# Kernel tuning notes

Hardware: AMD Instinct MI355X
Metric: run time of the kernel (lower is better)

Reference implementation:

```python
import math
import jax, jax.numpy as jnp
import numpy as np

# Dimensions (scalar irreps: o3.Irreps('8x0e').dim == 8, FullyConnectedTensorProduct
# between scalar irreps reduces to a learned bilinear map with a 3D weight tensor)
N = 50000       # nodes
C = 4           # channel dim ('c' in the einsum 'nci,neio->nceo')
DI = 8          # irreps_in.dim
DE = 8          # irreps_edge_attr.dim (must equal DI for the einsum to typecheck)
DO = 8          # irreps_out.dim (must equal DI for lin2 to consume the messages)
DA = 16         # irreps_node_attr.dim
E = 400000      # edges
F_EDGE = 32     # number_of_edge_features
H = 64          # radial_neurons
NUM_NEIGHBORS = 8


def setup_inputs() -> dict:
    key = jax.random.key(0)
    ks = jax.random.split(key, 12)
    inv = lambda f: 1.0 / np.sqrt(f)
    return {
        "node_input": jax.random.normal(ks[0], (N, C, DI), jnp.float32),
        "node_attr": jax.random.normal(ks[1], (N, DA), jnp.float32),
        "edge_features": jax.random.normal(ks[2], (E, F_EDGE), jnp.float32),
        # bilinear tensor-product weights (sc, lin1, lin2)
        "W_sc": jax.random.normal(ks[3], (DI, DA, DO), jnp.float32) * inv(DI * DA),
        "W_lin1": jax.random.normal(ks[4], (DI, DA, DI), jnp.float32) * inv(DI * DA),
        "W_lin2": jax.random.normal(ks[5], (DO, DA, DO), jnp.float32) * inv(DO * DA),
        # radial MLP: Linear(F_EDGE,H) -> SiLU -> Linear(H, DI*DE*DO)
        "fc_w1": jax.random.normal(ks[6], (F_EDGE, H), jnp.float32) * inv(F_EDGE),
        "fc_b1": jnp.zeros((H,), jnp.float32),
        "fc_w2": jax.random.normal(ks[7], (H, DI * DE * DO), jnp.float32) * inv(H),
        "fc_b2": jnp.zeros((DI * DE * DO,), jnp.float32),
        "edge_src": jax.random.randint(ks[8], (E,), 0, N, jnp.int32),
        "edge_dst": jax.random.randint(ks[9], (E,), 0, N, jnp.int32),
    }


def reference(node_input, node_attr, edge_features, W_sc, W_lin1, W_lin2,
              fc_w1, fc_b1, fc_w2, fc_b2, edge_src, edge_dst):
    n_nodes = node_input.shape[0]
    # self-connection and input linear (bilinear in node feature & node attr)
    s = jnp.einsum('nci,na,iao->nco', node_input, node_attr, W_sc)      # [N,C,DO]
    x = jnp.einsum('nci,na,iaj->ncj', node_input, node_attr, W_lin1)    # [N,C,DI]
    # radial MLP -> per-edge weight tensor [E, DI, DE, DO]
    h = jax.nn.silu(edge_features @ fc_w1 + fc_b1)
    ef = (h @ fc_w2 + fc_b2).reshape(-1, DI, DE, DO)
    # gather by source, per-edge contraction (einsum 'nci,neio->nceo'):
    # contract x's irrep dim with ef axis 2, keep ef axis 1 as output dim d
    msg = jnp.einsum('eci,edio->ecdo', x[edge_src], ef)                 # [E,C,DI,DO]
    # scatter-add to destination nodes
    agg = jax.ops.segment_sum(msg, edge_dst, num_segments=n_nodes)      # [N,C,DI,DO]
    agg = agg / jnp.sqrt(jnp.asarray(NUM_NEIGHBORS, agg.dtype))
    # output linear on the last (irreps_out) axis
    x2 = jnp.einsum('ncdo,na,oap->ncdp', agg, node_attr, W_lin2)        # [N,C,DI,DO]
    c_s = math.sin(math.pi / 8.0)
    # fully-connected scalar-irrep TP -> output_mask is all ones -> c_x scalar
    c_x = math.cos(math.pi / 8.0)
    return c_s * s[:, :, None, :] + c_x * x2
```

## Files before the change

### kernel.cpp

```cpp
#include <hip/hip_runtime.h>
#include <math.h>

#define CC 4
#define FE 32
#define HH 64
#define EBS 256
#define KEXT 544
#define ASTR 69

typedef __attribute__((ext_vector_type(8))) short bf16x8;
typedef __attribute__((ext_vector_type(4))) float f32x4;

__device__ inline unsigned short f2bf(float f) {
    unsigned u = __float_as_uint(f);
    u += 0x7fffu + ((u >> 16) & 1u);
    return (unsigned short)(u >> 16);
}
__device__ inline float bf2f(unsigned short b) {
    return __uint_as_float(((unsigned)b) << 16);
}

__global__ __launch_bounds__(256) void k_nodeprep(
    const float* __restrict__ node_input, const float* __restrict__ node_attr,
    const float* __restrict__ W_lin1, const float* __restrict__ W_sc,
    const float* __restrict__ W_lin2,
    float* __restrict__ xbuf, float* __restrict__ sbuf,
    float* __restrict__ w2n_ws, int N)
{
    const float c_s = 0.3826834323650898f;
    const float c_x_scaled = 0.9238795325112867f * 0.35355339059327373f;
    int node = blockIdx.x * 4 + (threadIdx.x >> 6);
    int lane = threadIdx.x & 63;
    if (node >= N) return;

    float attr_own = (lane < 16) ? node_attr[(size_t)node * 16 + lane] : 0.f;
    float ni_own   = (lane < 32) ? node_input[(size_t)node * 32 + lane] : 0.f;

    int iw = lane >> 3, jw = lane & 7;
    float wb1 = 0.f, wbs = 0.f, w2n = 0.f;
    #pragma unroll
    for (int a = 0; a < 16; ++a) {
        float fa = __shfl(attr_own, a);
        int idx = (iw * 16 + a) * 8 + jw;
        wb1 += fa * W_lin1[idx];
        wbs += fa * W_sc[idx];
        w2n += fa * W_lin2[idx];
    }
    w2n_ws[(size_t)node * 64 + lane] = c_x_scaled * w2n;

    int c_ = (lane >> 3) & 3, jo = lane & 7;
    float xo = 0.f, so = 0.f;
    #pragma unroll
    for (int i = 0; i < 8; ++i) {
        float niv = __shfl(ni_own, c_ * 8 + i);
        xo += niv * __shfl(wb1, i * 8 + jo);
        so += niv * __shfl(wbs, i * 8 + jo);
    }
    if (lane < 32) {
        xbuf[(size_t)node * 32 + lane] = xo;
        sbuf[(size_t)node * 32 + lane] = c_s * so;
    }
}

__global__ __launch_bounds__(256) void k_hist(
    const int* __restrict__ edge_dst, int* __restrict__ counts, int E)
{
    int e = blockIdx.x * 256 + threadIdx.x;
    if (e < E) atomicAdd(&counts[edge_dst[e]], 1);
}

__global__ __launch_bounds__(1024) void k_scan(
    const int* __restrict__ counts, int* __restrict__ offsets,
    int* __restrict__ cursor, int N)
{
    __shared__ int wsum[16];
    __shared__ int wpre[16];
    __shared__ int s_tot;
    __shared__ int s_carry;
    int tid = threadIdx.x, wid = tid >> 6, lane = tid & 63;
    if (tid == 0) s_carry = 0;
    __syncthreads();
    for (int base = 0; base < N; base += 1024) {
        int idx = base + tid;
        int v = (idx < N) ? counts[idx] : 0;
        int x = v;
        #pragma unroll
        for (int s = 1; s < 64; s <<= 1) {
            int y = __shfl_up(x, s);
            if (lane >= s) x += y;
        }
        if (lane == 63) wsum[wid] = x;
        __syncthreads();
        if (wid == 0) {
            int wv = (lane < 16) ? wsum[lane] : 0;
            int wx = wv;
            #pragma unroll
            for (int s = 1; s < 16; s <<= 1) {
                int y = __shfl_up(wx, s);
                if (lane >= s) wx += y;
            }
            if (lane < 16) wpre[lane] = wx - wv;
            if (lane == 15) s_tot = wx;
        }
        __syncthreads();
        if (idx < N) {
            int excl = s_carry + wpre[wid] + (x - v);
            offsets[idx] = excl;
            cursor[idx] = excl;
        }
        __syncthreads();
        if (tid == 0) s_carry += s_tot;
    }
}

__global__ __launch_bounds__(256) void k_fill(
    const int* __restrict__ edge_dst, const int* __restrict__ edge_src,
    int* __restrict__ cursor, int2* __restrict__ esrc, int E)
{
    int e = blockIdx.x * 256 + threadIdx.x;
    if (e < E) {
        int pos = atomicAdd(&cursor[edge_dst[e]], 1);
        int2 v; v.x = e; v.y = edge_src[e];
        esrc[pos] = v;
    }
}

__global__ __launch_bounds__(256) void k_prep_bfrag(
    const float* __restrict__ fc_w2, const float* __restrict__ fc_b2,
    unsigned short* __restrict__ Bfrag)
{
    int t = blockIdx.x * 256 + threadIdx.x;
    if (t >= KEXT * 64) return;
    int kappa = t >> 6, nu = t & 63;
    int d = nu >> 3, o = nu & 7;
    float val;
    if (kappa < 512)      val = fc_w2[(size_t)(kappa >> 3) * 512 + d * 64 + (kappa & 7) * 8 + o];
    else if (kappa < 520) val = fc_b2[d * 64 + (kappa & 7) * 8 + o];
    else                  val = 0.f;
    int kk = kappa >> 5;
    int lane = ((kappa >> 3) & 3) * 16 + (nu & 15);
    int ct = nu >> 4;
    int j = kappa & 7;
    Bfrag[(size_t)((kk * 4 + ct) * 64 + lane) * 8 + j] = f2bf(val);
}

__global__ __launch_bounds__(256) void k_prep_bfrag1(
    const float* __restrict__ fc_w1, unsigned short* __restrict__ Bfrag1)
{
    int t = blockIdx.x * 256 + threadIdx.x;
    if (t >= 4 * 64 * 8) return;
    int j = t & 7, l = (t >> 3) & 63, ct = t >> 9;
    int k = (l >> 4) * 8 + j;
    int n = ct * 16 + (l & 15);
    Bfrag1[t] = f2bf(fc_w1[(size_t)k * HH + n]);
}

__global__ __launch_bounds__(256) void k_hsilu(
    const float* __restrict__ edge_features,
    const unsigned short* __restrict__ Bfrag1, const float* __restrict__ fc_b1,
    unsigned short* __restrict__ H, int E)
{
    int wid = threadIdx.x >> 6, lane = threadIdx.x & 63;
    int e0 = (blockIdx.x * 4 + wid) * 16;
    if (e0 >= E) return;

    bf16x8 b[4];
    #pragma unroll
    for (int ct = 0; ct < 4; ++ct) {
        uint4 bv = reinterpret_cast<const uint4*>(Bfrag1)[ct * 64 + lane];
        b[ct] = *reinterpret_cast<bf16x8*>(&bv);
    }
    float bias[4];
    #pragma unroll
    for (int ct = 0; ct < 4; ++ct) bias[ct] = fc_b1[ct * 16 + (lane & 15)];

    int row = e0 + (lane & 15);
    if (row >= E) row = E - 1;
    const float4* ap = reinterpret_cast<const float4*>(
        edge_features + (size_t)row * FE + (lane >> 4) * 8);
    float4 a0 = ap[0], a1 = ap[1];
    unsigned au[4];
    au[0] = (unsigned)f2bf(a0.x) | ((unsigned)f2bf(a0.y) << 16);
    au[1] = (unsigned)f2bf(a0.z) | ((unsigned)f2bf(a0.w) << 16);
    au[2] = (unsigned)f2bf(a1.x) | ((unsigned)f2bf(a1.y) << 16);
    au[3] = (unsigned)f2bf(a1.z) | ((unsigned)f2bf(a1.w) << 16);
    bf16x8 a = *reinterpret_cast<bf16x8*>(au);

    f32x4 acc[4];
    #pragma unroll
    for (int ct = 0; ct < 4; ++ct) {
        acc[ct] = (f32x4){0.f, 0.f, 0.f, 0.f};
        acc[ct] = __builtin_amdgcn_mfma_f32_16x16x32_bf16(a, b[ct], acc[ct], 0, 0, 0);
    }

    #pragma unroll
    for (int ct = 0; ct < 4; ++ct) {
        #pragma unroll
        for (int v = 0; v < 4; ++v) {
            int r = e0 + (lane >> 4) * 4 + v;
            if (r < E) {
                float x = acc[ct][v] + bias[ct];
                float s = x / (1.f + __expf(-x));
                H[(size_t)r * HH + ct * 16 + (lane & 15)] = f2bf(s);
            }
        }
    }
}

__global__ __launch_bounds__(256) void k_zgemm(
    const unsigned short* __restrict__ H, const int2* __restrict__ esrc,
    const int* __restrict__ offsets, const int* __restrict__ counts,
    const float* __restrict__ xin, const unsigned short* __restrict__ Bfrag,
    float* __restrict__ out, int N)
{
    __shared__ uint4 alds[16 * ASTR];
    int wid = threadIdx.x >> 6, lane = threadIdx.x & 63;
    int node = blockIdx.x * 4 + wid;
    bool valid = (node < N);

    float z[CC][8];
    #pragma unroll
    for (int c = 0; c < CC; ++c)
        #pragma unroll
        for (int i = 0; i < 8; ++i) z[c][i] = 0.f;
    float xsown = 0.f;

    int off = 0, cnt = 0;
    if (valid) { off = offsets[node]; cnt = counts[node]; }
    for (int base = 0; base < cnt; base += 64) {
        int m = (cnt - base < 64) ? (cnt - base) : 64;
        int2 ej = (lane < m) ? esrc[off + base + lane] : make_int2(0, 0);
        #pragma unroll 2
        for (int j = 0; j < m; ++j) {
            int e   = __shfl(ej.x, j);
            int src = __shfl(ej.y, j);
            float hk = bf2f(H[(size_t)e * HH + lane]);
            const float4* xp = reinterpret_cast<const float4*>(xin + (size_t)src * 32);
            float xs[32];
            #pragma unroll
            for (int q = 0; q < 8; ++q) {
                float4 v = xp[q];
                xs[q * 4 + 0] = v.x; xs[q * 4 + 1] = v.y;
                xs[q * 4 + 2] = v.z; xs[q * 4 + 3] = v.w;
            }
            #pragma unroll
            for (int c = 0; c < CC; ++c)
                #pragma unroll
                for (int i = 0; i < 8; ++i)
                    z[c][i] += hk * xs[c * 8 + i];
            xsown += xin[(size_t)src * 32 + (lane & 31)];
        }
    }

    #pragma unroll
    for (int c = 0; c < CC; ++c) {
        uint4 pk;
        pk.x = (unsigned)f2bf(z[c][0]) | ((unsigned)f2bf(z[c][1]) << 16);
        pk.y = (unsigned)f2bf(z[c][2]) | ((unsigned)f2bf(z[c][3]) << 16);
        pk.z = (unsigned)f2bf(z[c][4]) | ((unsigned)f2bf(z[c][5]) << 16);
        pk.w = (unsigned)f2bf(z[c][6]) | ((unsigned)f2bf(z[c][7]) << 16);
        alds[(wid * 4 + c) * ASTR + lane] = pk;
    }
    float xb[8];
    #pragma unroll
    for (int i = 0; i < 8; ++i) xb[i] = __shfl(xsown, (lane & 3) * 8 + i);
    int r4 = wid * 4;
    if (lane < 4) {
        uint4 pk;
        pk.x = (unsigned)f2bf(xb[0]) | ((unsigned)f2bf(xb[1]) << 16);
        pk.y = (unsigned)f2bf(xb[2]) | ((unsigned)f2bf(xb[3]) << 16);
        pk.z = (unsigned)f2bf(xb[4]) | ((unsigned)f2bf(xb[5]) << 16);
        pk.w = (unsigned)f2bf(xb[6]) | ((unsigned)f2bf(xb[7]) << 16);
        alds[(r4 + lane) * ASTR + 64] = pk;
    } else if (lane < 16) {
        int j = lane - 4;
        uint4 zz; zz.x = 0u; zz.y = 0u; zz.z = 0u; zz.w = 0u;
        alds[(r4 + (j & 3)) * ASTR + 65 + (j >> 2)] = zz;
    }

    bf16x8 bfr[17];
    #pragma unroll
    for (int kk = 0; kk < 16; ++kk) {
        uint4 bv = reinterpret_cast<const uint4*>(Bfrag)[(kk * 4 + wid) * 64 + lane];
        bfr[kk] = *reinterpret_cast<bf16x8*>(&bv);
    }
    {
        uint4 bv = reinterpret_cast<const uint4*>(Bfrag)[(64 + wid) * 64 + lane];
        bfr[16] = *reinterpret_cast<bf16x8*>(&bv);
    }

    __syncthreads();

    f32x4 acc = (f32x4){0.f, 0.f, 0.f, 0.f};
    #pragma unroll
    for (int kk = 0; kk < 16; ++kk) {
        uint4 av = alds[(lane & 15) * ASTR + kk * 4 + (lane >> 4)];
        bf16x8 a = *reinterpret_cast<bf16x8*>(&av);
        acc = __builtin_amdgcn_mfma_f32_16x16x32_bf16(a, bfr[kk], acc, 0, 0, 0);
    }
    {
        uint4 av = alds[(lane & 15) * ASTR + 64 + (lane >> 4)];
        bf16x8 a = *reinterpret_cast<bf16x8*>(&av);
        acc = __builtin_amdgcn_mfma_f32_16x16x32_bf16(a, bfr[16], acc, 0, 0, 0);
    }

    int rbase = blockIdx.x * 16;
    int M = N * 4;
    #pragma unroll
    for (int v = 0; v < 4; ++v) {
        int r = rbase + (lane >> 4) * 4 + v;
        if (r < M)
            out[(size_t)r * 64 + wid * 16 + (lane & 15)] = acc[v];
    }
}

__global__ __launch_bounds__(256) void k_node_out(
    const float* __restrict__ sbuf, const float* __restrict__ w2n_ws,
    float* __restrict__ out, int N)
{
    int node = blockIdx.x * 4 + (threadIdx.x >> 6);
    int lane = threadIdx.x & 63;
    if (node >= N) return;
    int d = lane >> 3, p = lane & 7;

    float w2 = w2n_ws[(size_t)node * 64 + lane];
    float s_own = sbuf[(size_t)node * 32 + (lane & 31)];

    float w2sh[8];
    #pragma unroll
    for (int o = 0; o < 8; ++o) w2sh[o] = __shfl(w2, o * 8 + p);

    float* rowp = out + (size_t)node * 256;
    #pragma unroll
    for (int c = 0; c < CC; ++c) {
        float a_own = rowp[c * 64 + lane];
        float res = 0.f;
        #pragma unroll
        for (int o = 0; o < 8; ++o)
            res += __shfl(a_own, d * 8 + o) * w2sh[o];
        float sval = __shfl(s_own, c * 8 + p);
        rowp[c * 64 + lane] = sval + res;
    }
}

__global__ __launch_bounds__(EBS) void k_edge_atomic(
    const float* __restrict__ edge_features,
    const float* __restrict__ fc_w1, const float* __restrict__ fc_b1,
    const float* __restrict__ fc_w2, const float* __restrict__ fc_b2,
    const int* __restrict__ edge_src, const int* __restrict__ edge_dst,
    const float* __restrict__ xin, float* __restrict__ agg, int E)
{
    __shared__ float hlds[HH * EBS];
    int e = blockIdx.x * EBS + threadIdx.x;
    if (e >= E) return;
    float h[HH];
    #pragma unroll
    for (int k = 0; k < HH; ++k) h[k] = fc_b1[k];
    const float4* efp = reinterpret_cast<const float4*>(edge_features + (size_t)e * FE);
    #pragma unroll
    for (int fq = 0; fq < FE / 4; ++fq) {
        float4 efv = efp[fq];
        float ev[4] = {efv.x, efv.y, efv.z, efv.w};
        #pragma unroll
        for (int fs = 0; fs < 4; ++fs) {
            float evv = ev[fs];
            const float4* w1p = reinterpret_cast<const float4*>(fc_w1 + (fq * 4 + fs) * HH);
            #pragma unroll
            for (int q = 0; q < HH / 4; ++q) {
                float4 w = w1p[q];
                h[q * 4 + 0] += evv * w.x;
                h[q * 4 + 1] += evv * w.y;
                h[q * 4 + 2] += evv * w.z;
                h[q * 4 + 3] += evv * w.w;
            }
        }
    }
    #pragma unroll
    for (int k = 0; k < HH; ++k) {
        float v = h[k];
        hlds[k * EBS + threadIdx.x] = v / (1.f + __expf(-v));
    }
    int src = edge_src[e], dst = edge_dst[e];
    float xs[32];
    const float4* xp = reinterpret_cast<const float4*>(xin + (size_t)src * 32);
    #pragma unroll
    for (int q = 0; q < 8; ++q) {
        float4 v = xp[q];
        xs[q * 4 + 0] = v.x; xs[q * 4 + 1] = v.y;
        xs[q * 4 + 2] = v.z; xs[q * 4 + 3] = v.w;
    }
    float* outp = agg + (size_t)dst * 256;
    #pragma unroll 1
    for (int d = 0; d < 8; ++d) {
        float t[64];
        const float4* b2p = reinterpret_cast<const float4*>(fc_b2 + d * 64);
        #pragma unroll
        for (int q = 0; q < 16; ++q) {
            float4 v = b2p[q];
            t[q * 4 + 0] = v.x; t[q * 4 + 1] = v.y;
            t[q * 4 + 2] = v.z; t[q * 4 + 3] = v.w;
        }
        for (int k = 0; k < HH; ++k) {
            float hv = hlds[k * EBS + threadIdx.x];
            const float4* wp = reinterpret_cast<const float4*>(fc_w2 + (size_t)k * 512 + d * 64);
            #pragma unroll
            for (int q = 0; q < 16; ++q) {
                float4 w = wp[q];
                t[q * 4 + 0] += hv * w.x;
                t[q * 4 + 1] += hv * w.y;
                t[q * 4 + 2] += hv * w.z;
                t[q * 4 + 3] += hv * w.w;
            }
        }
        #pragma unroll
        for (int c = 0; c < CC; ++c) {
            #pragma unroll
            for (int o = 0; o < 8; ++o) {
                float acc = 0.f;
                #pragma unroll
                for (int i = 0; i < 8; ++i) acc += xs[c * 8 + i] * t[i * 8 + o];
                atomicAdd(outp + c * 64 + d * 8 + o, acc);
            }
        }
    }
}

extern "C" void kernel_launch(void* const* d_in, const int* in_sizes, int n_in,
                              void* d_out, int out_size, void* d_ws, size_t ws_size,
                              hipStream_t stream)
{
    const float* node_input    = (const float*)d_in[0];
    const float* node_attr     = (const float*)d_in[1];
    const float* edge_features = (const float*)d_in[2];
    const float* W_sc          = (const float*)d_in[3];
    const float* W_lin1        = (const float*)d_in[4];
    const float* W_lin2        = (const float*)d_in[5];
    const float* fc_w1         = (const float*)d_in[6];
    const float* fc_b1         = (const float*)d_in[7];
    const float* fc_w2         = (const float*)d_in[8];
    const float* fc_b2         = (const float*)d_in[9];
    const int*   edge_src      = (const int*)d_in[10];
    const int*   edge_dst      = (const int*)d_in[11];

    const int N = in_sizes[1] / 16;
    const int E = in_sizes[10];

    char* ws = (char*)d_ws;
    size_t off = 0;
    auto take = [&](size_t bytes) { char* p = ws + off; off += (bytes + 15) & ~(size_t)15; return p; };
    float* xbuf            = (float*)take((size_t)N * 32 * sizeof(float));
    float* sbuf            = (float*)take((size_t)N * 32 * sizeof(float));
    float* w2n_ws          = (float*)take((size_t)N * 64 * sizeof(float));
    int*   counts          = (int*)take((size_t)N * sizeof(int));
    int*   offsets         = (int*)take((size_t)N * sizeof(int));
    int*   cursor          = (int*)take((size_t)N * sizeof(int));
    int2*  esrc            = (int2*)take((size_t)E * sizeof(int2));
    unsigned short* Bfrag  = (unsigned short*)take((size_t)17 * 4 * 64 * 8 * sizeof(unsigned short));
    unsigned short* Bfrag1 = (unsigned short*)take((size_t)4 * 64 * 8 * sizeof(unsigned short));
    unsigned short* Hbuf   = (unsigned short*)take((size_t)E * HH * sizeof(unsigned short));
    bool fast = (off <= ws_size);

    float* out = (float*)d_out;

    k_nodeprep<<<(N + 3) / 4, 256, 0, stream>>>(
        node_input, node_attr, W_lin1, W_sc, W_lin2, xbuf, sbuf, w2n_ws, N);

    if (fast) {
        hipMemsetAsync(counts, 0, (size_t)N * sizeof(int), stream);
        k_hist<<<(E + 255) / 256, 256, 0, stream>>>(edge_dst, counts, E);
        k_scan<<<1, 1024, 0, stream>>>(counts, offsets, cursor, N);
        k_fill<<<(E + 255) / 256, 256, 0, stream>>>(edge_dst, edge_src, cursor, esrc, E);
        k_prep_bfrag1<<<(4 * 64 * 8 + 255) / 256, 256, 0, stream>>>(fc_w1, Bfrag1);
        k_prep_bfrag<<<(KEXT * 64 + 255) / 256, 256, 0, stream>>>(fc_w2, fc_b2, Bfrag);
        k_hsilu<<<(E + 63) / 64, 256, 0, stream>>>(edge_features, Bfrag1, fc_b1, Hbuf, E);
        k_zgemm<<<(N + 3) / 4, 256, 0, stream>>>(
            Hbuf, esrc, offsets, counts, xbuf, Bfrag, out, N);
    } else {
        hipMemsetAsync(d_out, 0, (size_t)out_size * sizeof(float), stream);
        k_edge_atomic<<<(E + EBS - 1) / EBS, EBS, 0, stream>>>(
            edge_features, fc_w1, fc_b1, fc_w2, fc_b2, edge_src, edge_dst, xbuf, out, E);
    }

    k_node_out<<<(N + 3) / 4, 256, 0, stream>>>(sbuf, w2n_ws, out, N);
}
```

Measured before the change: 315.1 us.

## Parallelize scan, degree-sort nodes, batch edge loads, fuse output linear into zgemm

Replaces the single-block serial scan with a three-phase multi-block scan, and adds a degree histogram so nodes are permuted by in-degree, which balances work across the waves in a zgemm block. The zgemm inner loop now batches eight edges' H loads and reads source rows through scalar (readfirstlane) addresses to raise memory-level parallelism. The lin2 and self-connection epilogue is fused into zgemm, removing the separate k_node_out pass and a full round-trip of the output through memory. In exchange it adds several small kernel launches and scattered output writes through the node permutation.

```diff
diff --git a/kernel.cpp b/kernel.cpp
--- a/kernel.cpp
+++ b/kernel.cpp
@@ -69,47 +69,104 @@
     if (e < E) atomicAdd(&counts[edge_dst[e]], 1);
 }
 
-__global__ __launch_bounds__(1024) void k_scan(
+__global__ __launch_bounds__(1024) void k_scanA(
     const int* __restrict__ counts, int* __restrict__ offsets,
-    int* __restrict__ cursor, int N)
+    int* __restrict__ btot, int N)
 {
     __shared__ int wsum[16];
     __shared__ int wpre[16];
-    __shared__ int s_tot;
-    __shared__ int s_carry;
     int tid = threadIdx.x, wid = tid >> 6, lane = tid & 63;
-    if (tid == 0) s_carry = 0;
+    int idx = blockIdx.x * 1024 + tid;
+    int v = (idx < N) ? counts[idx] : 0;
+    int x = v;
+    #pragma unroll
+    for (int s = 1; s < 64; s <<= 1) {
+        int y = __shfl_up(x, s);
+        if (lane >= s) x += y;
+    }
+    if (lane == 63) wsum[wid] = x;
     __syncthreads();
-    for (int base = 0; base < N; base += 1024) {
-        int idx = base + tid;
-        int v = (idx < N) ? counts[idx] : 0;
-        int x = v;
-        #pragma unroll
-        for (int s = 1; s < 64; s <<= 1) {
-            int y = __shfl_up(x, s);
-            if (lane >= s) x += y;
-        }
-        if (lane == 63) wsum[wid] = x;
-        __syncthreads();
-        if (wid == 0) {
-            int wv = (lane < 16) ? wsum[lane] : 0;
-            int wx = wv;
-            #pragma unroll
-            for (int s = 1; s < 16; s <<= 1) {
-                int y = __shfl_up(wx, s);
-                if (lane >= s) wx += y;
-            }
-            if (lane < 16) wpre[lane] = wx - wv;
-            if (lane == 15) s_tot = wx;
-        }
-        __syncthreads();
-        if (idx < N) {
-            int excl = s_carry + wpre[wid] + (x - v);
-            offsets[idx] = excl;
-            cursor[idx] = excl;
-        }
-        __syncthreads();
-        if (tid == 0) s_carry += s_tot;
+    if (wid == 0) {
+        int wv = (lane < 16) ? wsum[lane] : 0;
+        int wx = wv;
+        #pragma unroll
+        for (int s = 1; s < 16; s <<= 1) {
+            int y = __shfl_up(wx, s);
+            if (lane >= s) wx += y;
+        }
+        if (lane < 16) wpre[lane] = wx - wv;
+    }
+    __syncthreads();
+    int excl = wpre[wid] + (x - v);
+    if (idx < N) offsets[idx] = excl;
+    if (tid == 1023) btot[blockIdx.x] = excl + v;
+}
+
+__global__ __launch_bounds__(1024) void k_scanB(int* __restrict__ btot, int nb)
+{
+    __shared__ int wsum[16];
+    __shared__ int wpre[16];
+    int tid = threadIdx.x, wid = tid >> 6, lane = tid & 63;
+    int v = (tid < nb) ? btot[tid] : 0;
+    int x = v;
+    #pragma unroll
+    for (int s = 1; s < 64; s <<= 1) {
+        int y = __shfl_up(x, s);
+        if (lane >= s) x += y;
+    }
+    if (lane == 63) wsum[wid] = x;
+    __syncthreads();
+    if (wid == 0) {
+        int wv = (lane < 16) ? wsum[lane] : 0;
+        int wx = wv;
+        #pragma unroll
+        for (int s = 1; s < 16; s <<= 1) {
+            int y = __shfl_up(wx, s);
+            if (lane >= s) wx += y;
+        }
+        if (lane < 16) wpre[lane] = wx - wv;
+    }
+    __syncthreads();
+    if (tid < nb) btot[tid] = wpre[wid] + (x - v);
+}
+
+__global__ __launch_bounds__(256) void k_scanC(
+    int* __restrict__ offsets, const int* __restrict__ btot,
+    int* __restrict__ cursor, const int* __restrict__ counts,
+    int* __restrict__ dh, int N)
+{
+    int i = blockIdx.x * 256 + threadIdx.x;
+    if (i < N) {
+        int o = offsets[i] + btot[i >> 10];
+        offsets[i] = o;
+        cursor[i] = o;
+        int b = counts[i]; if (b > 63) b = 63;
+        atomicAdd(&dh[b], 1);
+    }
+}
+
+__global__ __launch_bounds__(64) void k_dscan(int* __restrict__ dh)
+{
+    int lane = threadIdx.x;
+    int v = dh[lane];
+    int x = v;
+    #pragma unroll
+    for (int s = 1; s < 64; s <<= 1) {
+        int y = __shfl_up(x, s);
+        if (lane >= s) x += y;
+    }
+    dh[lane] = x - v;
+}
+
+__global__ __launch_bounds__(256) void k_dscatter(
+    const int* __restrict__ counts, int* __restrict__ dcur,
+    int* __restrict__ nodeperm, int N)
+{
+    int i = blockIdx.x * 256 + threadIdx.x;
+    if (i < N) {
+        int b = counts[i]; if (b > 63) b = 63;
+        int pos = atomicAdd(&dcur[b], 1);
+        nodeperm[pos] = i;
     }
 }
 
@@ -210,13 +267,16 @@
 __global__ __launch_bounds__(256) void k_zgemm(
     const unsigned short* __restrict__ H, const int2* __restrict__ esrc,
     const int* __restrict__ offsets, const int* __restrict__ counts,
+    const int* __restrict__ nodeperm,
     const float* __restrict__ xin, const unsigned short* __restrict__ Bfrag,
+    const float* __restrict__ sbuf, const float* __restrict__ w2n_ws,
     float* __restrict__ out, int N)
 {
     __shared__ uint4 alds[16 * ASTR];
     int wid = threadIdx.x >> 6, lane = threadIdx.x & 63;
-    int node = blockIdx.x * 4 + wid;
-    bool valid = (node < N);
+    int nidx_w = blockIdx.x * 4 + wid;
+    bool valid = (nidx_w < N);
+    int node = valid ? nodeperm[nidx_w] : 0;
 
     float z[CC][8];
     #pragma unroll
@@ -230,25 +290,30 @@
     for (int base = 0; base < cnt; base += 64) {
         int m = (cnt - base < 64) ? (cnt - base) : 64;
         int2 ej = (lane < m) ? esrc[off + base + lane] : make_int2(0, 0);
-        #pragma unroll 2
-        for (int j = 0; j < m; ++j) {
-            int e   = __shfl(ej.x, j);
-            int src = __shfl(ej.y, j);
-            float hk = bf2f(H[(size_t)e * HH + lane]);
-            const float4* xp = reinterpret_cast<const float4*>(xin + (size_t)src * 32);
-            float xs[32];
+        for (int cb = 0; cb < m; cb += 8) {
+            int mm = m - cb; if (mm > 8) mm = 8;
+            float hk[8];
+            int   ssrc[8];
             #pragma unroll
-            for (int q = 0; q < 8; ++q) {
-                float4 v = xp[q];
-                xs[q * 4 + 0] = v.x; xs[q * 4 + 1] = v.y;
-                xs[q * 4 + 2] = v.z; xs[q * 4 + 3] = v.w;
+            for (int t = 0; t < 8; ++t) {
+                int jj = cb + (t < mm ? t : 0);
+                int e  = __shfl(ej.x, jj);
+                ssrc[t] = __builtin_amdgcn_readfirstlane(__shfl(ej.y, jj));
+                hk[t]  = bf2f(H[(size_t)e * HH + lane]);
             }
             #pragma unroll
-            for (int c = 0; c < CC; ++c)
-                #pragma unroll
-                for (int i = 0; i < 8; ++i)
-                    z[c][i] += hk * xs[c * 8 + i];
-            xsown += xin[(size_t)src * 32 + (lane & 31)];
+            for (int t = 0; t < 8; ++t) {
+                if (t < mm) {
+                    const float* xr = xin + (size_t)ssrc[t] * 32;
+                    float h = hk[t];
+                    #pragma unroll
+                    for (int c = 0; c < CC; ++c)
+                        #pragma unroll
+                        for (int i = 0; i < 8; ++i)
+                            z[c][i] += h * xr[c * 8 + i];
+                    xsown += xin[(size_t)ssrc[t] * 32 + (lane & 31)];
+                }
+            }
         }
     }
 
@@ -304,13 +369,28 @@
         acc = __builtin_amdgcn_mfma_f32_16x16x32_bf16(a, bfr[16], acc, 0, 0, 0);
     }
 
-    int rbase = blockIdx.x * 16;
-    int M = N * 4;
+    int q = lane >> 4;
+    int colc = lane & 15;
+    int nidx_q = blockIdx.x * 4 + q;
+    bool vq = (nidx_q < N);
+    int realn = vq ? nodeperm[nidx_q] : 0;
+    int col = wid * 16 + colc;
+    int p = col & 7;
+    int dloc8 = (colc >> 3) << 3;
+    float w2r[8];
+    #pragma unroll
+    for (int o = 0; o < 8; ++o)
+        w2r[o] = vq ? w2n_ws[(size_t)realn * 64 + o * 8 + p] : 0.f;
     #pragma unroll
     for (int v = 0; v < 4; ++v) {
-        int r = rbase + (lane >> 4) * 4 + v;
-        if (r < M)
-            out[(size_t)r * 64 + wid * 16 + (lane & 15)] = acc[v];
+        float res = 0.f;
+        #pragma unroll
+        for (int o = 0; o < 8; ++o)
+            res += __shfl(acc[v], q * 16 + dloc8 + o) * w2r[o];
+        if (vq) {
+            float sv = sbuf[(size_t)realn * 32 + v * 8 + p];
+            out[(size_t)(realn * 4 + v) * 64 + col] = sv + res;
+        }
     }
 }
 
@@ -444,6 +524,7 @@
 
     const int N = in_sizes[1] / 16;
     const int E = in_sizes[10];
+    const int nb = (N + 1023) / 1024;
 
     char* ws = (char*)d_ws;
     size_t off = 0;
@@ -452,13 +533,16 @@
     float* sbuf            = (float*)take((size_t)N * 32 * sizeof(float));
     float* w2n_ws          = (float*)take((size_t)N * 64 * sizeof(float));
     int*   counts          = (int*)take((size_t)N * sizeof(int));
+    int*   dh              = (int*)take((size_t)64 * sizeof(int));
     int*   offsets         = (int*)take((size_t)N * sizeof(int));
     int*   cursor          = (int*)take((size_t)N * sizeof(int));
+    int*   btot            = (int*)take((size_t)1024 * sizeof(int));
+    int*   nodeperm        = (int*)take((size_t)N * sizeof(int));
     int2*  esrc            = (int2*)take((size_t)E * sizeof(int2));
     unsigned short* Bfrag  = (unsigned short*)take((size_t)17 * 4 * 64 * 8 * sizeof(unsigned short));
     unsigned short* Bfrag1 = (unsigned short*)take((size_t)4 * 64 * 8 * sizeof(unsigned short));
     unsigned short* Hbuf   = (unsigned short*)take((size_t)E * HH * sizeof(unsigned short));
-    bool fast = (off <= ws_size);
+    bool fast = (off <= ws_size) && (((size_t)N * 32) % 16 == 0);
 
     float* out = (float*)d_out;
 
@@ -466,20 +550,23 @@
         node_input, node_attr, W_lin1, W_sc, W_lin2, xbuf, sbuf, w2n_ws, N);
 
     if (fast) {
-        hipMemsetAsync(counts, 0, (size_t)N * sizeof(int), stream);
+        hipMemsetAsync(counts, 0, ((size_t)N + 64) * sizeof(int), stream);
         k_hist<<<(E + 255) / 256, 256, 0, stream>>>(edge_dst, counts, E);
-        k_scan<<<1, 1024, 0, stream>>>(counts, offsets, cursor, N);
+        k_scanA<<<nb, 1024, 0, stream>>>(counts, offsets, btot, N);
+        k_scanB<<<1, 1024, 0, stream>>>(btot, nb);
+        k_scanC<<<(N + 255) / 256, 256, 0, stream>>>(offsets, btot, cursor, counts, dh, N);
+        k_dscan<<<1, 64, 0, stream>>>(dh);
+        k_dscatter<<<(N + 255) / 256, 256, 0, stream>>>(counts, dh, nodeperm, N);
         k_fill<<<(E + 255) / 256, 256, 0, stream>>>(edge_dst, edge_src, cursor, esrc, E);
         k_prep_bfrag1<<<(4 * 64 * 8 + 255) / 256, 256, 0, stream>>>(fc_w1, Bfrag1);
         k_prep_bfrag<<<(KEXT * 64 + 255) / 256, 256, 0, stream>>>(fc_w2, fc_b2, Bfrag);
         k_hsilu<<<(E + 63) / 64, 256, 0, stream>>>(edge_features, Bfrag1, fc_b1, Hbuf, E);
         k_zgemm<<<(N + 3) / 4, 256, 0, stream>>>(
-            Hbuf, esrc, offsets, counts, xbuf, Bfrag, out, N);
+            Hbuf, esrc, offsets, counts, nodeperm, xbuf, Bfrag, sbuf, w2n_ws, out, N);
     } else {
         hipMemsetAsync(d_out, 0, (size_t)out_size * sizeof(float), stream);
         k_edge_atomic<<<(E + EBS - 1) / EBS, EBS, 0, stream>>>(
             edge_features, fc_w1, fc_b1, fc_w2, fc_b2, edge_src, edge_dst, xbuf, out, E);
-    }
-
-    k_node_out<<<(N + 3) / 4, 256, 0, stream>>>(sbuf, w2n_ws, out, N);
-}
+        k_node_out<<<(N + 3) / 4, 256, 0, stream>>>(sbuf, w2n_ws, out, N);
+    }
+}
```

Measured after the change: 570.0 us. +80.9%, slower.
